# Performance work log

Measured on AMD Instinct MI355X. Metric: run time of the kernel, lower is better.

Reference implementation:

```python
import jax, jax.numpy as jnp
import numpy as np

SHARPNESS = 2.0
EPS = 1e-12  # F.normalize default eps


def _l2norm_c(x):
    # L2-normalize along channel axis (axis=1), matching F.normalize(dim=1)
    n = jnp.sqrt(jnp.sum(x * x, axis=1, keepdims=True))
    return x / jnp.maximum(n, EPS)


def setup_inputs() -> dict:
    key = jax.random.key(0)
    k1, k2, k3 = jax.random.split(key, 3)
    N, C, H, W_ = 16, 256, 56, 56
    feat = jax.random.normal(k1, (N, C, H, W_), dtype=jnp.float32)
    W = jax.random.normal(k2, (C, C), dtype=jnp.float32) * 0.05  # 1x1 conv weight [out,in]
    b = jax.random.normal(k3, (C,), dtype=jnp.float32) * 0.05
    return {"feat": feat, "W": W, "b": b}


def reference(feat, W, b):
    N, C, H, W_ = feat.shape
    HW = H * W_
    # 1x1 conv == channel matmul
    feat_value = jnp.einsum('nchw,oc->nohw', feat, W) + b[None, :, None, None]
    feat_value = _l2norm_c(feat_value).reshape(N, C, HW)
    f = _l2norm_c(feat).reshape(N, C, HW)
    # correlation attention [N, HW, HW]
    attention = jnp.einsum('ncp,ncq->npq', f, f)
    attention = jnp.clip(attention, 0.0) ** SHARPNESS
    # bmm(feat_value, attention.transpose(1,2)) -> out[n,c,p] = sum_q fv[n,c,q] * att[n,p,q]
    out = jnp.einsum('ncq,npq->ncp', feat_value, attention)
    return out.reshape(N, C, H, W_)
```

## Files before the change

kernel.cpp:

```cpp
#include <hip/hip_runtime.h>

typedef unsigned short u16;
typedef unsigned int u32;
typedef __attribute__((ext_vector_type(8))) short short8;
typedef __attribute__((ext_vector_type(8))) u16 u16x8;
typedef __attribute__((ext_vector_type(4))) u32 u32x4;
typedef __attribute__((ext_vector_type(4))) float f32x4;

#define NB 16
#define CC 256
#define HW 3136
#define NT 49

__device__ __forceinline__ u16 f2bf(float x) {
  u32 u = __float_as_uint(x);
  u += 0x7fffu + ((u >> 16) & 1u);
  return (u16)(u >> 16);
}

__device__ __forceinline__ f32x4 mfma16(short8 a, short8 b, f32x4 c) {
  return __builtin_amdgcn_mfma_f32_16x16x32_bf16(a, b, c, 0, 0, 0);
}

__device__ __forceinline__ void gl_lds16(const void* g, void* l) {
  __builtin_amdgcn_global_load_lds(
      (const __attribute__((address_space(1))) void*)g,
      (__attribute__((address_space(3))) void*)l, 16, 0, 0);
}

__global__ __launch_bounds__(256) void k_cvtw(const float* __restrict__ W,
                                              u16* __restrict__ Wbf) {
  int i = (blockIdx.x * 256 + threadIdx.x) * 4;
  f32x4 v = *(const f32x4*)(W + i);
  u32 lo = (u32)f2bf(v[0]) | ((u32)f2bf(v[1]) << 16);
  u32 hi = (u32)f2bf(v[2]) | ((u32)f2bf(v[3]) << 16);
  *(u32*)(Wbf + i) = lo;
  *(u32*)(Wbf + i + 2) = hi;
}

__global__ __launch_bounds__(256) void k_prep_f(const float* __restrict__ feat,
                                                u16* __restrict__ f_bf,
                                                float* __restrict__ norm_f) {
  int pt = blockIdx.x, n = blockIdx.y;
  int tid = threadIdx.x;
  __shared__ float tile[256][65];
  __shared__ float rinv[64];
  const float* src = feat + (size_t)n * CC * HW + pt * 64;
  int p = tid & 63;
  #pragma unroll 8
  for (int c = tid >> 6; c < 256; c += 4)
    tile[c][p] = src[(size_t)c * HW + p];
  __syncthreads();
  if (tid < 64) {
    float s = 0.f;
    #pragma unroll 16
    for (int c = 0; c < 256; ++c) { float v = tile[c][tid]; s += v * v; }
    float nv = fmaxf(sqrtf(s), 1e-12f);
    rinv[tid] = 1.0f / nv;
    norm_f[n * HW + pt * 64 + tid] = nv;
  }
  __syncthreads();
  u16* dst = f_bf + ((size_t)n * HW + pt * 64) * 256;
  #pragma unroll
  for (int j = 0; j < 8; ++j) {
    int chunk = j * 256 + tid;
    int pp = chunk >> 5;
    int c0 = (chunk & 31) * 8;
    float inv = rinv[pp];
    u16x8 o;
    #pragma unroll
    for (int k = 0; k < 8; ++k) o[k] = f2bf(tile[c0 + k][pp] * inv);
    *(u16x8*)(dst + pp * 256 + c0) = o;
  }
}

__global__ __launch_bounds__(256) void k_conv(const u16* __restrict__ Wbf,
                                              const float* __restrict__ bias,
                                              const u16* __restrict__ f_bf,
                                              const float* __restrict__ norm_f,
                                              u16* __restrict__ fv_bf) {
  int qt = blockIdx.x, n = blockIdx.y;
  int tid = threadIdx.x;
  int lane = tid & 63, w = tid >> 6;
  int lr = lane & 15, lg = lane >> 4;
  __shared__ __align__(16) char fq[32768];
  __shared__ float wred[4][64];
  __shared__ float sinv[64];

  const char* fsrc = (const char*)(f_bf + ((size_t)n * HW + qt * 64) * 256);
  #pragma unroll
  for (int rep = 0; rep < 8; ++rep) {
    int linear = rep * 4096 + tid * 16;
    int q = linear >> 9;
    int cb = linear & 0x1F0;
    u32x4 v = *(const u32x4*)(fsrc + q * 512 + cb);
    *(u32x4*)(fq + q * 512 + (cb ^ ((q & 7) << 4))) = v;
  }
  __syncthreads();

  f32x4 acc[4][4] = {};
  #pragma unroll
  for (int kk = 0; kk < 8; ++kk) {
    short8 bfr[4], afr[4];
    #pragma unroll
    for (int j = 0; j < 4; ++j) {
      int q = j * 16 + lr;
      bfr[j] = *(const short8*)(fq + q * 512 + ((kk * 64 + lg * 16) ^ ((q & 7) << 4)));
    }
    #pragma unroll
    for (int i = 0; i < 4; ++i) {
      int o = w * 64 + i * 16 + lr;
      afr[i] = *(const short8*)((const char*)Wbf + (size_t)o * 512 + kk * 64 + lg * 16);
    }
    #pragma unroll
    for (int i = 0; i < 4; ++i)
      #pragma unroll
      for (int j = 0; j < 4; ++j)
        acc[i][j] = mfma16(afr[i], bfr[j], acc[i][j]);
  }

  float nf[4];
  #pragma unroll
  for (int j = 0; j < 4; ++j) nf[j] = norm_f[n * HW + qt * 64 + j * 16 + lr];
  float partial[4] = {0.f, 0.f, 0.f, 0.f};
  #pragma unroll
  for (int i = 0; i < 4; ++i)
    #pragma unroll
    for (int r = 0; r < 4; ++r) {
      float bv = bias[w * 64 + i * 16 + lg * 4 + r];
      #pragma unroll
      for (int j = 0; j < 4; ++j) {
        float pre = acc[i][j][r] * nf[j] + bv;
        acc[i][j][r] = pre;
        partial[j] += pre * pre;
      }
    }
  #pragma unroll
  for (int j = 0; j < 4; ++j) {
    float v = partial[j];
    v += __shfl_xor(v, 16);
    v += __shfl_xor(v, 32);
    if (lane < 16) wred[w][j * 16 + lane] = v;
  }
  __syncthreads();
  if (tid < 64) {
    float s = wred[0][tid] + wred[1][tid] + wred[2][tid] + wred[3][tid];
    sinv[tid] = 1.0f / fmaxf(sqrtf(s), 1e-12f);
  }
  __syncthreads();
  u16* dst = fv_bf + (size_t)n * CC * HW + qt * 64;
  #pragma unroll
  for (int i = 0; i < 4; ++i)
    #pragma unroll
    for (int r = 0; r < 4; ++r) {
      int o = w * 64 + i * 16 + lg * 4 + r;
      #pragma unroll
      for (int j = 0; j < 4; ++j) {
        int q = j * 16 + lr;
        dst[(size_t)o * HW + q] = f2bf(acc[i][j][r] * sinv[q]);
      }
    }
}

__global__ __launch_bounds__(256, 2) void k_attn(const u16* __restrict__ f_bf,
                                                 const u16* __restrict__ fv_bf,
                                                 float* __restrict__ out) {
  int linear = blockIdx.y * NT + blockIdx.x;
  int vb = (linear & 7) * 98 + (linear >> 3);
  int n = vb / NT;
  int pt = vb - n * NT;

  int tid = threadIdx.x;
  int lane = tid & 63, w = tid >> 6;
  int lr = lane & 15, lg = lane >> 4;
  int wp = w & 1, wq = w >> 1;
  __shared__ __align__(16) char fqd[2][32768];
  __shared__ __align__(16) char attl[8192];

  const char* fbase = (const char*)f_bf + (size_t)n * HW * 512;
  const char* fvbase = (const char*)fv_bf + (size_t)n * CC * HW * 2;

  int so[8];
  #pragma unroll
  for (int r = 0; r < 8; ++r) {
    int q = w * 16 + r * 2 + (lane >> 5);
    int col = (lane & 31) * 16;
    so[r] = q * 512 + (col ^ ((q & 7) << 4));
  }

  short8 ap[2][8];
  #pragma unroll
  for (int fi = 0; fi < 2; ++fi) {
    int p = pt * 64 + wp * 32 + fi * 16 + lr;
    #pragma unroll
    for (int kk = 0; kk < 8; ++kk)
      ap[fi][kk] = *(const short8*)(fbase + (size_t)p * 512 + kk * 64 + lg * 16);
  }

  #pragma unroll
  for (int r = 0; r < 8; ++r)
    gl_lds16(fbase + so[r], (char*)fqd[0] + (w * 8 + r) * 1024);

  f32x4 oacc[4][4] = {};

  for (int qt = 0; qt < NT; ++qt) {
    const char* fq = fqd[qt & 1];

    asm volatile("s_waitcnt vmcnt(0)" ::: "memory");
    __builtin_amdgcn_sched_barrier(0);
    __builtin_amdgcn_s_barrier();
    __builtin_amdgcn_sched_barrier(0);

    short8 av[2][4];
    #pragma unroll
    for (int kk = 0; kk < 2; ++kk)
      #pragma unroll
      for (int fi = 0; fi < 4; ++fi) {
        const char* pa = fvbase + (size_t)(w * 64 + fi * 16 + lr) * (HW * 2)
                         + qt * 128 + kk * 64 + lg * 16;
        asm volatile("global_load_dwordx4 %0, %1, off"
                     : "=&v"(av[kk][fi]) : "v"(pa) : "memory");
      }

    if (qt + 1 < NT) {
      const char* fsrc = fbase + (size_t)(qt + 1) * 32768;
      char* dbuf = (char*)fqd[(qt + 1) & 1];
      #pragma unroll
      for (int r = 0; r < 8; ++r)
        gl_lds16(fsrc + so[r], dbuf + (w * 8 + r) * 1024);
    }

    f32x4 s[2][2] = {};
    #pragma unroll
    for (int kk = 0; kk < 8; ++kk) {
      short8 bq[2];
      #pragma unroll
      for (int fj = 0; fj < 2; ++fj) {
        int q = wq * 32 + fj * 16 + lr;
        bq[fj] = *(const short8*)(fq + q * 512 + ((kk * 64 + lg * 16) ^ ((q & 7) << 4)));
      }
      s[0][0] = mfma16(ap[0][kk], bq[0], s[0][0]);
      s[0][1] = mfma16(ap[0][kk], bq[1], s[0][1]);
      s[1][0] = mfma16(ap[1][kk], bq[0], s[1][0]);
      s[1][1] = mfma16(ap[1][kk], bq[1], s[1][1]);
    }

    #pragma unroll
    for (int fi = 0; fi < 2; ++fi)
      #pragma unroll
      for (int fj = 0; fj < 2; ++fj)
        #pragma unroll
        for (int r = 0; r < 4; ++r) {
          float v = s[fi][fj][r];
          v = fmaxf(v, 0.f);
          v = v * v;
          int p = wp * 32 + fi * 16 + lg * 4 + r;
          int q = wq * 32 + fj * 16 + lr;
          *(u16*)(attl + p * 128 + ((q * 2) ^ ((p & 7) << 4))) = f2bf(v);
        }
    asm volatile("s_waitcnt lgkmcnt(0)" ::: "memory");
    __builtin_amdgcn_sched_barrier(0);
    __builtin_amdgcn_s_barrier();
    __builtin_amdgcn_sched_barrier(0);

    if (qt + 1 < NT) {
      asm volatile("s_waitcnt vmcnt(8)" ::: "memory");
    } else {
      asm volatile("s_waitcnt vmcnt(0)" ::: "memory");
    }
    __builtin_amdgcn_sched_barrier(0);

    #pragma unroll
    for (int kk = 0; kk < 2; ++kk) {
      short8 bt[4];
      #pragma unroll
      for (int fp = 0; fp < 4; ++fp) {
        int p = fp * 16 + lr;
        bt[fp] = *(const short8*)(attl + p * 128 + ((kk * 64 + lg * 16) ^ ((p & 7) << 4)));
      }
      #pragma unroll
      for (int fi = 0; fi < 4; ++fi)
        #pragma unroll
        for (int fp = 0; fp < 4; ++fp)
          oacc[fi][fp] = mfma16(av[kk][fi], bt[fp], oacc[fi][fp]);
    }
  }

  float* op = out + (size_t)n * CC * HW + pt * 64;
  #pragma unroll
  for (int fi = 0; fi < 4; ++fi)
    #pragma unroll
    for (int r = 0; r < 4; ++r) {
      int c = w * 64 + fi * 16 + lg * 4 + r;
      #pragma unroll
      for (int fp = 0; fp < 4; ++fp)
        op[(size_t)c * HW + fp * 16 + lr] = oacc[fi][fp][r];
    }
}

extern "C" void kernel_launch(void* const* d_in, const int* in_sizes, int n_in,
                              void* d_out, int out_size, void* d_ws, size_t ws_size,
                              hipStream_t stream) {
  const float* feat = (const float*)d_in[0];
  const float* W    = (const float*)d_in[1];
  const float* bias = (const float*)d_in[2];
  float* out = (float*)d_out;

  char* ws = (char*)d_ws;
  u16*   Wbf    = (u16*)ws;
  float* norm_f = (float*)(ws + 131072);
  u16*   f_bf   = (u16*)(ws + 331776);
  u16*   fv_bf  = (u16*)(ws + 26021888);

  k_cvtw<<<dim3(64), dim3(256), 0, stream>>>(W, Wbf);
  k_prep_f<<<dim3(NT, NB), dim3(256), 0, stream>>>(feat, f_bf, norm_f);
  k_conv<<<dim3(NT, NB), dim3(256), 0, stream>>>(Wbf, bias, f_bf, norm_f, fv_bf);
  k_attn<<<dim3(NT, NB), dim3(256), 0, stream>>>(f_bf, fv_bf, out);
}
```

Before: 308.3 us.

## Halve q-tile to 32 in attention kernel to fit three blocks per CU

The attention kernel now walks the key dimension in 32-wide tiles (98 iterations) instead of 64-wide tiles. Each wave owns a 16-row slice of p instead of a 2x2 split. This shrinks shared memory from about 72KB to about 37KB per block and cuts register use (ap, av, s), so launch bounds can ask for 3 blocks per CU instead of 2. The attention staging buffer drops the XOR swizzle in favour of an 80-byte padded row. The trade-off is twice as many barrier and wait rounds per block, each with less MFMA work to hide latency behind.

```diff
diff --git a/kernel.cpp b/kernel.cpp
--- a/kernel.cpp
+++ b/kernel.cpp
@@ -11,6 +11,7 @@
 #define CC 256
 #define HW 3136
 #define NT 49
+#define NT2 98
 
 __device__ __forceinline__ u16 f2bf(float x) {
   u32 u = __float_as_uint(x);
@@ -162,7 +163,7 @@
     }
 }
 
-__global__ __launch_bounds__(256, 2) void k_attn(const u16* __restrict__ f_bf,
+__global__ __launch_bounds__(256, 3) void k_attn(const u16* __restrict__ f_bf,
                                                  const u16* __restrict__ fv_bf,
                                                  float* __restrict__ out) {
   int linear = blockIdx.y * NT + blockIdx.x;
@@ -173,37 +174,37 @@
   int tid = threadIdx.x;
   int lane = tid & 63, w = tid >> 6;
   int lr = lane & 15, lg = lane >> 4;
-  int wp = w & 1, wq = w >> 1;
-  __shared__ __align__(16) char fqd[2][32768];
-  __shared__ __align__(16) char attl[8192];
+  __shared__ __align__(16) char fqd[2][16384];
+  __shared__ __align__(16) char attl[5120];
 
   const char* fbase = (const char*)f_bf + (size_t)n * HW * 512;
   const char* fvbase = (const char*)fv_bf + (size_t)n * CC * HW * 2;
 
-  int so[8];
-  #pragma unroll
-  for (int r = 0; r < 8; ++r) {
-    int q = w * 16 + r * 2 + (lane >> 5);
+  int so[4];
+  #pragma unroll
+  for (int r = 0; r < 4; ++r) {
+    int q = w * 8 + r * 2 + (lane >> 5);
     int col = (lane & 31) * 16;
     so[r] = q * 512 + (col ^ ((q & 7) << 4));
   }
 
-  short8 ap[2][8];
-  #pragma unroll
-  for (int fi = 0; fi < 2; ++fi) {
-    int p = pt * 64 + wp * 32 + fi * 16 + lr;
-    #pragma unroll
-    for (int kk = 0; kk < 8; ++kk)
-      ap[fi][kk] = *(const short8*)(fbase + (size_t)p * 512 + kk * 64 + lg * 16);
-  }
-
-  #pragma unroll
-  for (int r = 0; r < 8; ++r)
-    gl_lds16(fbase + so[r], (char*)fqd[0] + (w * 8 + r) * 1024);
+  short8 ap[8];
+  #pragma unroll
+  for (int kk = 0; kk < 8; ++kk) {
+    const char* pa = fbase + (size_t)(pt * 64 + w * 16 + lr) * 512 + kk * 64 + lg * 16;
+    asm volatile("global_load_dwordx4 %0, %1, off"
+                 : "=&v"(ap[kk]) : "v"(pa) : "memory");
+  }
+  asm volatile("s_waitcnt vmcnt(0)" ::: "memory");
+  __builtin_amdgcn_sched_barrier(0);
+
+  #pragma unroll
+  for (int r = 0; r < 4; ++r)
+    gl_lds16(fbase + so[r], (char*)fqd[0] + (w * 4 + r) * 1024);
 
   f32x4 oacc[4][4] = {};
 
-  for (int qt = 0; qt < NT; ++qt) {
+  for (int qt = 0; qt < NT2; ++qt) {
     const char* fq = fqd[qt & 1];
 
     asm volatile("s_waitcnt vmcnt(0)" ::: "memory");
@@ -211,79 +212,68 @@
     __builtin_amdgcn_s_barrier();
     __builtin_amdgcn_sched_barrier(0);
 
-    short8 av[2][4];
-    #pragma unroll
-    for (int kk = 0; kk < 2; ++kk)
-      #pragma unroll
-      for (int fi = 0; fi < 4; ++fi) {
-        const char* pa = fvbase + (size_t)(w * 64 + fi * 16 + lr) * (HW * 2)
-                         + qt * 128 + kk * 64 + lg * 16;
-        asm volatile("global_load_dwordx4 %0, %1, off"
-                     : "=&v"(av[kk][fi]) : "v"(pa) : "memory");
-      }
-
-    if (qt + 1 < NT) {
-      const char* fsrc = fbase + (size_t)(qt + 1) * 32768;
+    short8 av[4];
+    #pragma unroll
+    for (int fi = 0; fi < 4; ++fi) {
+      const char* pa = fvbase + (size_t)(w * 64 + fi * 16 + lr) * (HW * 2)
+                       + qt * 64 + lg * 16;
+      asm volatile("global_load_dwordx4 %0, %1, off"
+                   : "=&v"(av[fi]) : "v"(pa) : "memory");
+    }
+
+    if (qt + 1 < NT2) {
+      const char* fsrc = fbase + (size_t)(qt + 1) * 16384;
       char* dbuf = (char*)fqd[(qt + 1) & 1];
       #pragma unroll
-      for (int r = 0; r < 8; ++r)
-        gl_lds16(fsrc + so[r], dbuf + (w * 8 + r) * 1024);
-    }
-
-    f32x4 s[2][2] = {};
+      for (int r = 0; r < 4; ++r)
+        gl_lds16(fsrc + so[r], dbuf + (w * 4 + r) * 1024);
+    }
+
+    f32x4 s[2] = {};
     #pragma unroll
     for (int kk = 0; kk < 8; ++kk) {
       short8 bq[2];
       #pragma unroll
       for (int fj = 0; fj < 2; ++fj) {
-        int q = wq * 32 + fj * 16 + lr;
+        int q = fj * 16 + lr;
         bq[fj] = *(const short8*)(fq + q * 512 + ((kk * 64 + lg * 16) ^ ((q & 7) << 4)));
       }
-      s[0][0] = mfma16(ap[0][kk], bq[0], s[0][0]);
-      s[0][1] = mfma16(ap[0][kk], bq[1], s[0][1]);
-      s[1][0] = mfma16(ap[1][kk], bq[0], s[1][0]);
-      s[1][1] = mfma16(ap[1][kk], bq[1], s[1][1]);
-    }
-
-    #pragma unroll
-    for (int fi = 0; fi < 2; ++fi)
-      #pragma unroll
-      for (int fj = 0; fj < 2; ++fj)
-        #pragma unroll
-        for (int r = 0; r < 4; ++r) {
-          float v = s[fi][fj][r];
-          v = fmaxf(v, 0.f);
-          v = v * v;
-          int p = wp * 32 + fi * 16 + lg * 4 + r;
-          int q = wq * 32 + fj * 16 + lr;
-          *(u16*)(attl + p * 128 + ((q * 2) ^ ((p & 7) << 4))) = f2bf(v);
-        }
+      s[0] = mfma16(ap[kk], bq[0], s[0]);
+      s[1] = mfma16(ap[kk], bq[1], s[1]);
+    }
+
+    #pragma unroll
+    for (int fj = 0; fj < 2; ++fj)
+      #pragma unroll
+      for (int r = 0; r < 4; ++r) {
+        float v = s[fj][r];
+        v = fmaxf(v, 0.f);
+        v = v * v;
+        int p = w * 16 + lg * 4 + r;
+        int q = fj * 16 + lr;
+        *(u16*)(attl + p * 80 + q * 2) = f2bf(v);
+      }
     asm volatile("s_waitcnt lgkmcnt(0)" ::: "memory");
     __builtin_amdgcn_sched_barrier(0);
     __builtin_amdgcn_s_barrier();
     __builtin_amdgcn_sched_barrier(0);
 
-    if (qt + 1 < NT) {
-      asm volatile("s_waitcnt vmcnt(8)" ::: "memory");
+    if (qt + 1 < NT2) {
+      asm volatile("s_waitcnt vmcnt(4)" ::: "memory");
     } else {
       asm volatile("s_waitcnt vmcnt(0)" ::: "memory");
     }
     __builtin_amdgcn_sched_barrier(0);
 
-    #pragma unroll
-    for (int kk = 0; kk < 2; ++kk) {
-      short8 bt[4];
-      #pragma unroll
-      for (int fp = 0; fp < 4; ++fp) {
-        int p = fp * 16 + lr;
-        bt[fp] = *(const short8*)(attl + p * 128 + ((kk * 64 + lg * 16) ^ ((p & 7) << 4)));
-      }
-      #pragma unroll
-      for (int fi = 0; fi < 4; ++fi)
-        #pragma unroll
-        for (int fp = 0; fp < 4; ++fp)
-          oacc[fi][fp] = mfma16(av[kk][fi], bt[fp], oacc[fi][fp]);
-    }
+    short8 bt[4];
+    #pragma unroll
+    for (int fp = 0; fp < 4; ++fp)
+      bt[fp] = *(const short8*)(attl + (fp * 16 + lr) * 80 + lg * 16);
+    #pragma unroll
+    for (int fi = 0; fi < 4; ++fi)
+      #pragma unroll
+      for (int fp = 0; fp < 4; ++fp)
+        oacc[fi][fp] = mfma16(av[fi], bt[fp], oacc[fi][fp]);
   }
 
   float* op = out + (size_t)n * CC * HW + pt * 64;
```

Result: slower. 362.5 us (+17.6%).

## Prefetch feat_value tiles one iteration ahead with register double-buffering and setprio

Applied to the files above, without the earlier changes.

The loop over q-tiles is unrolled by two with ping-pong register buffers, so the feat_value A-operands for the next tile are loaded during the current tile's work instead of being loaded and waited on within the same iteration. The mid-iteration vmcnt wait goes away, and s_setprio raises wave priority around the MFMA sections. The cost is more VGPR pressure from the doubled operand buffers, which could lower occupancy. The top-of-loop vmcnt(0) now also waits for the prefetched loads.

```diff
diff --git a/kernel.cpp b/kernel.cpp
--- a/kernel.cpp
+++ b/kernel.cpp
@@ -16,6 +16,11 @@
   u32 u = __float_as_uint(x);
   u += 0x7fffu + ((u >> 16) & 1u);
   return (u16)(u >> 16);
+}
+
+__device__ __forceinline__ float relu2(float v) {
+  v = fmaxf(v, 0.f);
+  return v * v;
 }
 
 __device__ __forceinline__ f32x4 mfma16(short8 a, short8 b, f32x4 c) {
@@ -197,94 +202,106 @@
       ap[fi][kk] = *(const short8*)(fbase + (size_t)p * 512 + kk * 64 + lg * 16);
   }
 
+  short8 avA[2][4], avB[2][4];
+
   #pragma unroll
   for (int r = 0; r < 8; ++r)
     gl_lds16(fbase + so[r], (char*)fqd[0] + (w * 8 + r) * 1024);
+  #pragma unroll
+  for (int kk = 0; kk < 2; ++kk)
+    #pragma unroll
+    for (int fi = 0; fi < 4; ++fi)
+      avA[kk][fi] = *(const short8*)(fvbase +
+                      (size_t)(w * 64 + fi * 16 + lr) * (HW * 2) +
+                      kk * 64 + lg * 16);
 
   f32x4 oacc[4][4] = {};
 
-  for (int qt = 0; qt < NT; ++qt) {
-    const char* fq = fqd[qt & 1];
-
-    asm volatile("s_waitcnt vmcnt(0)" ::: "memory");
-    __builtin_amdgcn_sched_barrier(0);
-    __builtin_amdgcn_s_barrier();
-    __builtin_amdgcn_sched_barrier(0);
-
-    short8 av[2][4];
-    #pragma unroll
-    for (int kk = 0; kk < 2; ++kk)
-      #pragma unroll
-      for (int fi = 0; fi < 4; ++fi) {
-        const char* pa = fvbase + (size_t)(w * 64 + fi * 16 + lr) * (HW * 2)
-                         + qt * 128 + kk * 64 + lg * 16;
-        asm volatile("global_load_dwordx4 %0, %1, off"
-                     : "=&v"(av[kk][fi]) : "v"(pa) : "memory");
-      }
-
-    if (qt + 1 < NT) {
-      const char* fsrc = fbase + (size_t)(qt + 1) * 32768;
-      char* dbuf = (char*)fqd[(qt + 1) & 1];
-      #pragma unroll
-      for (int r = 0; r < 8; ++r)
-        gl_lds16(fsrc + so[r], dbuf + (w * 8 + r) * 1024);
-    }
-
-    f32x4 s[2][2] = {};
-    #pragma unroll
-    for (int kk = 0; kk < 8; ++kk) {
-      short8 bq[2];
-      #pragma unroll
-      for (int fj = 0; fj < 2; ++fj) {
-        int q = wq * 32 + fj * 16 + lr;
-        bq[fj] = *(const short8*)(fq + q * 512 + ((kk * 64 + lg * 16) ^ ((q & 7) << 4)));
-      }
-      s[0][0] = mfma16(ap[0][kk], bq[0], s[0][0]);
-      s[0][1] = mfma16(ap[0][kk], bq[1], s[0][1]);
-      s[1][0] = mfma16(ap[1][kk], bq[0], s[1][0]);
-      s[1][1] = mfma16(ap[1][kk], bq[1], s[1][1]);
-    }
-
-    #pragma unroll
-    for (int fi = 0; fi < 2; ++fi)
-      #pragma unroll
-      for (int fj = 0; fj < 2; ++fj)
-        #pragma unroll
-        for (int r = 0; r < 4; ++r) {
-          float v = s[fi][fj][r];
-          v = fmaxf(v, 0.f);
-          v = v * v;
-          int p = wp * 32 + fi * 16 + lg * 4 + r;
-          int q = wq * 32 + fj * 16 + lr;
-          *(u16*)(attl + p * 128 + ((q * 2) ^ ((p & 7) << 4))) = f2bf(v);
-        }
-    asm volatile("s_waitcnt lgkmcnt(0)" ::: "memory");
-    __builtin_amdgcn_sched_barrier(0);
-    __builtin_amdgcn_s_barrier();
-    __builtin_amdgcn_sched_barrier(0);
-
-    if (qt + 1 < NT) {
-      asm volatile("s_waitcnt vmcnt(8)" ::: "memory");
-    } else {
-      asm volatile("s_waitcnt vmcnt(0)" ::: "memory");
-    }
-    __builtin_amdgcn_sched_barrier(0);
-
-    #pragma unroll
-    for (int kk = 0; kk < 2; ++kk) {
-      short8 bt[4];
-      #pragma unroll
-      for (int fp = 0; fp < 4; ++fp) {
-        int p = fp * 16 + lr;
-        bt[fp] = *(const short8*)(attl + p * 128 + ((kk * 64 + lg * 16) ^ ((p & 7) << 4)));
-      }
-      #pragma unroll
-      for (int fi = 0; fi < 4; ++fi)
-        #pragma unroll
-        for (int fp = 0; fp < 4; ++fp)
-          oacc[fi][fp] = mfma16(av[kk][fi], bt[fp], oacc[fi][fp]);
-    }
-  }
+#define ABODY(AVC, AVN, QT, DOPF) do {                                        \
+    const char* fq_ = fqd[(QT) & 1];                                          \
+                               \
+    asm volatile("s_waitcnt vmcnt(0)" ::: "memory");                          \
+    __builtin_amdgcn_sched_barrier(0);                                        \
+    __builtin_amdgcn_s_barrier();                                             \
+    __builtin_amdgcn_sched_barrier(0);                                        \
+    if (DOPF) {                                                               \
+            \
+      const char* fsrc_ = fbase + (size_t)((QT) + 1) * 32768;                 \
+      char* dbuf_ = (char*)fqd[((QT) + 1) & 1];                               \
+      _Pragma("unroll")                                                       \
+      for (int r_ = 0; r_ < 8; ++r_)                                          \
+        gl_lds16(fsrc_ + so[r_], dbuf_ + (w * 8 + r_) * 1024);                \
+                         \
+      _Pragma("unroll")                                                       \
+      for (int kk_ = 0; kk_ < 2; ++kk_)                                       \
+        _Pragma("unroll")                                                     \
+        for (int fi_ = 0; fi_ < 4; ++fi_)                                     \
+          AVN[kk_][fi_] = *(const short8*)(fvbase +                           \
+                            (size_t)(w * 64 + fi_ * 16 + lr) * (HW * 2) +     \
+                            ((QT) + 1) * 128 + kk_ * 64 + lg * 16);           \
+    }                                                                         \
+                      \
+    f32x4 s_[2][2] = {};                                                      \
+    __builtin_amdgcn_s_setprio(1);                                            \
+    _Pragma("unroll")                                                         \
+    for (int kk_ = 0; kk_ < 8; ++kk_) {                                       \
+      short8 bq_[2];                                                          \
+      _Pragma("unroll")                                                       \
+      for (int fj_ = 0; fj_ < 2; ++fj_) {                                     \
+        int q_ = wq * 32 + fj_ * 16 + lr;                                     \
+        bq_[fj_] = *(const short8*)(fq_ + q_ * 512 +                          \
+                     ((kk_ * 64 + lg * 16) ^ ((q_ & 7) << 4)));               \
+      }                                                                       \
+      s_[0][0] = mfma16(ap[0][kk_], bq_[0], s_[0][0]);                        \
+      s_[0][1] = mfma16(ap[0][kk_], bq_[1], s_[0][1]);                        \
+      s_[1][0] = mfma16(ap[1][kk_], bq_[0], s_[1][0]);                        \
+      s_[1][1] = mfma16(ap[1][kk_], bq_[1], s_[1][1]);                        \
+    }                                                                         \
+    __builtin_amdgcn_s_setprio(0);                                            \
+                                               \
+    _Pragma("unroll")                                                         \
+    for (int fi_ = 0; fi_ < 2; ++fi_)                                         \
+      _Pragma("unroll")                                                       \
+      for (int fj_ = 0; fj_ < 2; ++fj_)                                       \
+        _Pragma("unroll")                                                     \
+        for (int r_ = 0; r_ < 4; ++r_) {                                      \
+          int p_ = wp * 32 + fi_ * 16 + lg * 4 + r_;                          \
+          int q_ = wq * 32 + fj_ * 16 + lr;                                   \
+          *(u16*)(attl + p_ * 128 + ((q_ * 2) ^ ((p_ & 7) << 4))) =           \
+              f2bf(relu2(s_[fi_][fj_][r_]));                                  \
+        }                                                                     \
+    asm volatile("s_waitcnt lgkmcnt(0)" ::: "memory");                        \
+    __builtin_amdgcn_sched_barrier(0);                                        \
+    __builtin_amdgcn_s_barrier();                                             \
+    __builtin_amdgcn_sched_barrier(0);                                        \
+        \
+    __builtin_amdgcn_s_setprio(1);                                            \
+    _Pragma("unroll")                                                         \
+    for (int kk_ = 0; kk_ < 2; ++kk_) {                                       \
+      short8 bt_[4];                                                          \
+      _Pragma("unroll")                                                       \
+      for (int fp_ = 0; fp_ < 4; ++fp_) {                                     \
+        int p_ = fp_ * 16 + lr;                                               \
+        bt_[fp_] = *(const short8*)(attl + p_ * 128 +                         \
+                     ((kk_ * 64 + lg * 16) ^ ((p_ & 7) << 4)));               \
+      }                                                                       \
+      _Pragma("unroll")                                                       \
+      for (int fi_ = 0; fi_ < 4; ++fi_)                                       \
+        _Pragma("unroll")                                                     \
+        for (int fp_ = 0; fp_ < 4; ++fp_)                                     \
+          oacc[fi_][fp_] = mfma16(AVC[kk_][fi_], bt_[fp_], oacc[fi_][fp_]);   \
+    }                                                                         \
+    __builtin_amdgcn_s_setprio(0);                                            \
+  } while (0)
+
+  #pragma unroll 1
+  for (int t = 0; t < 24; ++t) {
+    ABODY(avA, avB, 2 * t,     true);
+    ABODY(avB, avA, 2 * t + 1, true);
+  }
+  ABODY(avA, avB, 48, false);
+
+#undef ABODY
 
   float* op = out + (size_t)n * CC * HW + pt * 64;
   #pragma unroll
```

After: 531.5 us. +72.4%, slower.
